# Performance work log

Hardware: AMD Instinct MI355X
Metric: run time of the kernel (lower is better)

The kernel has to match this reference:

```python
import jax, jax.numpy as jnp
import numpy as np

HEADS = 8
DIM_HEAD = 64
MAX_REL = 200  # max_rel_dist


def setup_inputs() -> dict:
    key = jax.random.key(0)
    ks = jax.random.split(key, 5)
    B, N, D = 4, 2048, 512
    x = jax.random.normal(ks[0], (B, N, D), dtype=jnp.float32)
    temporal_mask = jax.random.randint(ks[1], (N, N), 0, 2, dtype=jnp.int32)
    gamma = jnp.ones((D,), jnp.float32)
    beta = jnp.zeros((D,), jnp.float32)
    Wqkv = jax.random.normal(ks[2], (D, 3 * HEADS * DIM_HEAD), dtype=jnp.float32) * 0.02
    Wout = jax.random.normal(ks[3], (HEADS * DIM_HEAD, D), dtype=jnp.float32) * 0.02
    bout = jnp.zeros((D,), jnp.float32)
    rel_table = jax.random.normal(ks[4], (2 * MAX_REL - 1,), dtype=jnp.float32) * 0.02
    return {"x": x, "gamma": gamma, "beta": beta, "Wqkv": Wqkv, "Wout": Wout,
            "bout": bout, "rel_table": rel_table, "temporal_mask": temporal_mask}


def reference(x, gamma, beta, Wqkv, Wout, bout, rel_table, temporal_mask):
    B, N, D = x.shape
    scale = DIM_HEAD ** -0.5
    # LayerNorm
    mu = jnp.mean(x, axis=-1, keepdims=True)
    var = jnp.mean(jnp.square(x - mu), axis=-1, keepdims=True)
    xn = (x - mu) * jax.lax.rsqrt(var + 1e-5) * gamma + beta
    # QKV projection (no bias), split heads: b n (h d) -> b h n d
    qkv = xn @ Wqkv  # [B, N, 3*H*d]
    q, k, v = jnp.split(qkv, 3, axis=-1)
    split = lambda t: t.reshape(B, N, HEADS, DIM_HEAD).transpose(0, 2, 1, 3)
    q, k, v = split(q), split(k), split(v)
    # scores with learned relative-position bias
    dots = jnp.einsum('bhnd,bhmd->bhnm', q, k) * scale  # [B,H,N,N]
    idx = jnp.arange(N)
    rel = jnp.clip(idx[:, None] - idx[None, :], -(MAX_REL - 1), MAX_REL - 1) + MAX_REL - 1
    dots = dots + rel_table[rel][None, None, :, :]
    # temporal mask (0 -> -inf); large negative for grad safety
    dots = jnp.where(temporal_mask[None, None, :, :] == 0, jnp.float32(-1e9), dots)
    attn = jax.nn.softmax(dots, axis=-1)
    out = jnp.einsum('bhnm,bhmd->bhnd', attn, v)
    out = out.transpose(0, 2, 1, 3).reshape(B, N, HEADS * DIM_HEAD)
    return out @ Wout + bout
```

## Files before the change

### kernel.cpp

```cpp
#include <hip/hip_runtime.h>

typedef __attribute__((ext_vector_type(8))) short bf16x8;
typedef __attribute__((ext_vector_type(4))) short bf16x4;
typedef __attribute__((ext_vector_type(4))) float f32x4;
typedef unsigned short ushort_t;

#define B_ 4
#define H_ 8
#define N_ 2048
#define D_ 512
#define MAXREL 199

__device__ __forceinline__ ushort_t f2bf(float f) {
    union { float f; unsigned u; } v; v.f = f;
    unsigned r = v.u + 0x7fffu + ((v.u >> 16) & 1u);
    return (ushort_t)(r >> 16);
}
__device__ __forceinline__ ushort_t f2bf_fast(float f) {
    union { float f; unsigned u; } v; v.f = f;
    return (ushort_t)((v.u + 0x8000u) >> 16);
}
__device__ __forceinline__ float bf2f(ushort_t u) {
    union { unsigned u; float f; } v; v.u = ((unsigned)u) << 16;
    return v.f;
}
__device__ __forceinline__ void gl_lds16(const ushort_t* g, ushort_t* l) {
    __builtin_amdgcn_global_load_lds(
        (const __attribute__((address_space(1))) void*)g,
        (__attribute__((address_space(3))) void*)l,
        16, 0, 0);
}

#define PREP_BIAS  16384
#define PREP_LN    8192
#define PREP_WQ    768
#define PREP_WO    256
__global__ __launch_bounds__(256) void prep_kernel(const float* __restrict__ x,
                                                   const float* __restrict__ gamma,
                                                   const float* __restrict__ beta,
                                                   ushort_t* __restrict__ xn,
                                                   const float* __restrict__ Wqkv,
                                                   ushort_t* __restrict__ WqkvT,
                                                   const float* __restrict__ Wout,
                                                   ushort_t* __restrict__ WoutT,
                                                   const float* __restrict__ rel,
                                                   const int* __restrict__ mask,
                                                   ushort_t* __restrict__ bp) {
    __shared__ float smem[32 * 33];
    const int blk = blockIdx.x;
    const int t = threadIdx.x;

    if (blk < PREP_BIAS) {
        int idx = blk * 256 + t;
        int n = idx >> 11, m = idx & 2047;
        int dl = n - m;
        dl = dl < -MAXREL ? -MAXREL : (dl > MAXREL ? MAXREL : dl);
        float v = (mask[idx] == 0) ? -1e9f : rel[dl + MAXREL];
        int jt = m >> 6, m16 = m & 15, nt = (m >> 4) & 3;
        bp[((size_t)n * 32 + jt) * 64 + m16 * 4 + nt] = f2bf(v);
    } else if (blk < PREP_BIAS + PREP_LN) {
        const int row = blk - PREP_BIAS;
        const float* xr = x + (size_t)row * D_;
        float v0 = xr[t];
        float v1 = xr[t + 256];
        float s = v0 + v1;
        for (int o = 32; o > 0; o >>= 1) s += __shfl_down(s, o);
        if ((t & 63) == 0) smem[t >> 6] = s;
        __syncthreads();
        float mu = (smem[0] + smem[1] + smem[2] + smem[3]) * (1.0f / D_);
        __syncthreads();
        float d0 = v0 - mu, d1 = v1 - mu;
        float s2 = d0 * d0 + d1 * d1;
        for (int o = 32; o > 0; o >>= 1) s2 += __shfl_down(s2, o);
        if ((t & 63) == 0) smem[t >> 6] = s2;
        __syncthreads();
        float var = (smem[0] + smem[1] + smem[2] + smem[3]) * (1.0f / D_);
        float rs = rsqrtf(var + 1e-5f);
        ushort_t* yr = xn + (size_t)row * D_;
        yr[t]       = f2bf(d0 * rs * gamma[t]       + beta[t]);
        yr[t + 256] = f2bf(d1 * rs * gamma[t + 256] + beta[t + 256]);
    } else {
        const float* W; ushort_t* Wt; int Nn, i;
        if (blk < PREP_BIAS + PREP_LN + PREP_WQ) {
            i = blk - (PREP_BIAS + PREP_LN); W = Wqkv; Wt = WqkvT; Nn = 1536;
        } else {
            i = blk - (PREP_BIAS + PREP_LN + PREP_WQ); W = Wout; Wt = WoutT; Nn = 512;
        }
        const int nb = Nn >> 5;
        const int bx = (i % nb) * 32, by = (i / nb) * 32;
        const int tx = t & 31, ty = t >> 5;
        float (*tile)[33] = (float(*)[33])smem;
        #pragma unroll
        for (int k = 0; k < 32; k += 8)
            tile[ty + k][tx] = W[(size_t)(by + ty + k) * Nn + bx + tx];
        __syncthreads();
        #pragma unroll
        for (int k = 0; k < 32; k += 8)
            Wt[(size_t)(bx + ty + k) * 512 + by + tx] = f2bf(tile[tx][ty + k]);
    }
}

__global__ __launch_bounds__(256) void gemm_qkv(const ushort_t* __restrict__ A,
                                                const ushort_t* __restrict__ Bt,
                                                ushort_t* __restrict__ qb,
                                                ushort_t* __restrict__ kb,
                                                ushort_t* __restrict__ vb) {
    __shared__ ushort_t As[128 * 32];
    __shared__ ushort_t Bs[128 * 32];
    const int t = threadIdx.x;
    const int lane = t & 63, w = t >> 6;
    const int m16 = lane & 15, quad = lane >> 4;
    const int wr = w >> 1, wc = w & 1;
    const int r0 = blockIdx.y * 128, c0 = blockIdx.x * 128;

    const ushort_t* Ag = A  + (size_t)(r0 + (t >> 2)) * D_ + (t & 3) * 8;
    const ushort_t* Bg = Bt + (size_t)(c0 + (t >> 2)) * D_ + (t & 3) * 8;
    ushort_t* AsW = As + w * 512;
    ushort_t* BsW = Bs + w * 512;

    f32x4 acc[4][4];
    #pragma unroll
    for (int i = 0; i < 4; i++)
        #pragma unroll
        for (int j = 0; j < 4; j++) acc[i][j] = (f32x4){0.f, 0.f, 0.f, 0.f};

    for (int k0 = 0; k0 < D_; k0 += 32) {
        gl_lds16(Ag + k0, AsW);
        gl_lds16(Ag + k0 + (size_t)64 * D_, AsW + 2048);
        gl_lds16(Bg + k0, BsW);
        gl_lds16(Bg + k0 + (size_t)64 * D_, BsW + 2048);
        __syncthreads();
        bf16x8 af[4], bfr[4];
        #pragma unroll
        for (int rt = 0; rt < 4; rt++)
            af[rt] = *(const bf16x8*)(As + (wr * 64 + rt * 16 + m16) * 32 + quad * 8);
        #pragma unroll
        for (int ct = 0; ct < 4; ct++)
            bfr[ct] = *(const bf16x8*)(Bs + (wc * 64 + ct * 16 + m16) * 32 + quad * 8);
        #pragma unroll
        for (int rt = 0; rt < 4; rt++)
            #pragma unroll
            for (int ct = 0; ct < 4; ct++)
                acc[rt][ct] = __builtin_amdgcn_mfma_f32_16x16x32_bf16(af[rt], bfr[ct], acc[rt][ct], 0, 0, 0);
        __syncthreads();
    }

    #pragma unroll
    for (int ct = 0; ct < 4; ct++) {
        int cc = c0 + wc * 64 + ct * 16;
        int which = cc >> 9;
        int h = (cc >> 6) & 7;
        int d = (cc & 63) + m16;
        #pragma unroll
        for (int rt = 0; rt < 4; rt++) {
            int rowb = r0 + wr * 64 + rt * 16 + quad * 4;
            int b = rowb >> 11, n0 = rowb & 2047;
            if (which == 0) {
                #pragma unroll
                for (int r = 0; r < 4; r++)
                    qb[((size_t)((b * H_ + h) * N_ + n0 + r)) * 64 + d] = f2bf(acc[rt][ct][r] * 0.125f);
            } else if (which == 1) {
                #pragma unroll
                for (int r = 0; r < 4; r++)
                    kb[((size_t)((b * H_ + h) * N_ + n0 + r)) * 64 + d] = f2bf(acc[rt][ct][r]);
            } else {
                union { ushort_t u4[4]; unsigned long long ll; } pk;
                #pragma unroll
                for (int r = 0; r < 4; r++) pk.u4[r] = f2bf(acc[rt][ct][r]);
                *(unsigned long long*)(vb + ((size_t)((b * H_ + h) * 64 + d)) * N_ + n0) = pk.ll;
            }
        }
    }
}

__global__ __launch_bounds__(256) void gemm_out(const ushort_t* __restrict__ A,
                                                const ushort_t* __restrict__ Bt,
                                                const float* __restrict__ bias,
                                                float* __restrict__ C) {
    __shared__ ushort_t As[64 * 32];
    __shared__ ushort_t Bs[128 * 32];
    const int t = threadIdx.x;
    const int lane = t & 63, w = t >> 6;
    const int m16 = lane & 15, quad = lane >> 4;
    const int wr = w >> 1, wc = w & 1;
    const int r0 = blockIdx.y * 64, c0 = blockIdx.x * 128;

    const ushort_t* Ag = A  + (size_t)(r0 + (t >> 2)) * D_ + (t & 3) * 8;
    const ushort_t* Bg = Bt + (size_t)(c0 + (t >> 2)) * D_ + (t & 3) * 8;
    ushort_t* AsW = As + w * 512;
    ushort_t* BsW = Bs + w * 512;

    f32x4 acc[2][4];
    #pragma unroll
    for (int i = 0; i < 2; i++)
        #pragma unroll
        for (int j = 0; j < 4; j++) acc[i][j] = (f32x4){0.f, 0.f, 0.f, 0.f};

    for (int k0 = 0; k0 < D_; k0 += 32) {
        gl_lds16(Ag + k0, AsW);
        gl_lds16(Bg + k0, BsW);
        gl_lds16(Bg + k0 + (size_t)64 * D_, BsW + 2048);
        __syncthreads();
        bf16x8 af[2], bfr[4];
        #pragma unroll
        for (int mf = 0; mf < 2; mf++)
            af[mf] = *(const bf16x8*)(As + (wr * 32 + mf * 16 + m16) * 32 + quad * 8);
        #pragma unroll
        for (int nt = 0; nt < 4; nt++)
            bfr[nt] = *(const bf16x8*)(Bs + (wc * 64 + nt * 16 + m16) * 32 + quad * 8);
        #pragma unroll
        for (int mf = 0; mf < 2; mf++)
            #pragma unroll
            for (int nt = 0; nt < 4; nt++)
                acc[mf][nt] = __builtin_amdgcn_mfma_f32_16x16x32_bf16(af[mf], bfr[nt], acc[mf][nt], 0, 0, 0);
        __syncthreads();
    }

    #pragma unroll
    for (int mf = 0; mf < 2; mf++) {
        #pragma unroll
        for (int nt = 0; nt < 4; nt++) {
            int col = c0 + wc * 64 + nt * 16 + m16;
            int row0 = r0 + wr * 32 + mf * 16 + quad * 4;
            float bv = bias[col];
            #pragma unroll
            for (int r = 0; r < 4; r++)
                C[(size_t)(row0 + r) * 512 + col] = acc[mf][nt][r] + bv;
        }
    }
}

__global__ __launch_bounds__(512, 4) void attn_mfma(const ushort_t* __restrict__ qb,
                                                    const ushort_t* __restrict__ kb,
                                                    const ushort_t* __restrict__ vb,
                                                    const ushort_t* __restrict__ bp,
                                                    ushort_t* __restrict__ attn) {
    __shared__ ushort_t Ks[2][64 * 64];
    __shared__ ushort_t Vs[2][64 * 64];
    __shared__ ushort_t p_s[8][16 * 64];

    const int t = threadIdx.x;
    const int w = t >> 6, lane = t & 63;
    const int m16 = lane & 15, quad = lane >> 4;
    const int id = blockIdx.x;
    const int bh = id & 31;
    const int qt = id >> 5;
    const int b = bh >> 3, h = bh & 7;
    const int n0w = qt * 128 + w * 16;

    const int srow = t >> 3, scb = t & 7;
    const int soff = srow * 64 + (scb ^ (srow & 7)) * 8;
    const ushort_t* kgbase = kb + ((size_t)bh * N_) * 64;
    const ushort_t* vgbase = vb + ((size_t)bh * 64) * N_;

    const ushort_t* qpb = qb + ((size_t)(bh * N_ + n0w + m16)) * 64 + quad * 8;
    bf16x8 qa0 = *(const bf16x8*)(qpb);
    bf16x8 qa1 = *(const bf16x8*)(qpb + 32);

    *(bf16x8*)(&Ks[0][soff]) = *(const bf16x8*)(kgbase + (size_t)srow * 64 + scb * 8);
    *(bf16x8*)(&Vs[0][soff]) = *(const bf16x8*)(vgbase + (size_t)srow * N_ + scb * 8);
    __syncthreads();

    f32x4 o[4];
    #pragma unroll
    for (int nt = 0; nt < 4; nt++) o[nt] = (f32x4){0.f, 0.f, 0.f, 0.f};
    float rsum[4] = {};

    for (int jt = 0; jt < 32; jt++) {
        const int buf = jt & 1;
        const int j0 = jt * 64;
        const bool more = (jt < 31);

        bf16x8 kst, vst;
        if (more) {
            kst = *(const bf16x8*)(kgbase + (size_t)(j0 + 64 + srow) * 64 + scb * 8);
            vst = *(const bf16x8*)(vgbase + (size_t)srow * N_ + j0 + 64 + scb * 8);
        }

        bf16x4 bcur[4];
        #pragma unroll
        for (int r = 0; r < 4; r++) {
            int n = n0w + quad * 4 + r;
            bcur[r] = *(const bf16x4*)(bp + ((size_t)n * 32 + jt) * 64 + m16 * 4);
        }

        f32x4 s[4];
        #pragma unroll
        for (int nt = 0; nt < 4; nt++) {
            int kr = nt * 16 + m16;
            bf16x8 kf0 = *(const bf16x8*)(&Ks[buf][kr * 64 + ((quad) ^ (kr & 7)) * 8]);
            bf16x8 kf1 = *(const bf16x8*)(&Ks[buf][kr * 64 + ((quad + 4) ^ (kr & 7)) * 8]);
            f32x4 a2 = (f32x4){0.f, 0.f, 0.f, 0.f};
            a2 = __builtin_amdgcn_mfma_f32_16x16x32_bf16(qa0, kf0, a2, 0, 0, 0);
            a2 = __builtin_amdgcn_mfma_f32_16x16x32_bf16(qa1, kf1, a2, 0, 0, 0);
            s[nt] = a2;
        }

        ushort_t* pw = p_s[w];
        #pragma unroll
        for (int nt = 0; nt < 4; nt++) {
            int chunk = nt * 2 + (m16 >> 3), pos = m16 & 7;
            #pragma unroll
            for (int r = 0; r < 4; r++) {
                float p = __expf(s[nt][r] + bf2f((ushort_t)bcur[r][nt]));
                rsum[r] += p;
                int row = quad * 4 + r;
                pw[row * 64 + ((chunk ^ (row & 7)) << 3) + pos] = f2bf_fast(p);
            }
        }

        bf16x8 pa0 = *(const bf16x8*)(pw + m16 * 64 + ((quad ^ (m16 & 7)) << 3));
        bf16x8 pa1 = *(const bf16x8*)(pw + m16 * 64 + (((quad + 4) ^ (m16 & 7)) << 3));

        #pragma unroll
        for (int nt = 0; nt < 4; nt++) {
            int d = nt * 16 + m16;
            bf16x8 vf0 = *(const bf16x8*)(&Vs[buf][d * 64 + ((quad) ^ (d & 7)) * 8]);
            bf16x8 vf1 = *(const bf16x8*)(&Vs[buf][d * 64 + ((quad + 4) ^ (d & 7)) * 8]);
            o[nt] = __builtin_amdgcn_mfma_f32_16x16x32_bf16(pa0, vf0, o[nt], 0, 0, 0);
            o[nt] = __builtin_amdgcn_mfma_f32_16x16x32_bf16(pa1, vf1, o[nt], 0, 0, 0);
        }

        if (more) {
            *(bf16x8*)(&Ks[buf ^ 1][soff]) = kst;
            *(bf16x8*)(&Vs[buf ^ 1][soff]) = vst;
        }
        __syncthreads();
    }

    #pragma unroll
    for (int r = 0; r < 4; r++) {
        float t2 = rsum[r];
        t2 += __shfl_xor(t2, 1);
        t2 += __shfl_xor(t2, 2);
        t2 += __shfl_xor(t2, 4);
        t2 += __shfl_xor(t2, 8);
        float inv = 1.0f / t2;
        int n = n0w + quad * 4 + r;
        ushort_t* orow = attn + ((size_t)(b * N_ + n)) * 512 + h * 64 + m16;
        #pragma unroll
        for (int nt = 0; nt < 4; nt++) orow[nt * 16] = f2bf(o[nt][r] * inv);
    }
}

extern "C" void kernel_launch(void* const* d_in, const int* in_sizes, int n_in,
                              void* d_out, int out_size, void* d_ws, size_t ws_size,
                              hipStream_t stream) {
    const float* x     = (const float*)d_in[0];
    const float* gamma = (const float*)d_in[1];
    const float* beta  = (const float*)d_in[2];
    const float* Wqkv  = (const float*)d_in[3];
    const float* Wout  = (const float*)d_in[4];
    const float* bout  = (const float*)d_in[5];
    const float* rel   = (const float*)d_in[6];
    const int*   mask  = (const int*)d_in[7];
    float* out = (float*)d_out;

    char* wsb = (char*)d_ws;
    ushort_t* xn    = (ushort_t*)(wsb);
    ushort_t* attnb = (ushort_t*)(wsb + ( 8u << 20));
    ushort_t* qb    = (ushort_t*)(wsb + (16u << 20));
    ushort_t* kb    = (ushort_t*)(wsb + (24u << 20));
    ushort_t* vb    = (ushort_t*)(wsb + (32u << 20));
    ushort_t* WqkvT = (ushort_t*)(wsb + (40u << 20));
    ushort_t* WoutT = (ushort_t*)(wsb + (42u << 20));
    ushort_t* bp    = (ushort_t*)(wsb + (44u << 20));

    prep_kernel<<<PREP_BIAS + PREP_LN + PREP_WQ + PREP_WO, 256, 0, stream>>>(
        x, gamma, beta, xn, Wqkv, WqkvT, Wout, WoutT, rel, mask, bp);

    gemm_qkv<<<dim3(1536 / 128, 8192 / 128), 256, 0, stream>>>(xn, WqkvT, qb, kb, vb);

    attn_mfma<<<512, 512, 0, stream>>>(qb, kb, vb, bp, attnb);

    gemm_out<<<dim3(512 / 128, 8192 / 64), 256, 0, stream>>>(attnb, WoutT, bout, out);
}
```

Measured before the change: 198.6 us.

## Compute transposed scores, pass probabilities via shuffles instead of LDS, use exp2

After: 210.6 us. 6.1% more time.

```diff
diff --git a/kernel.cpp b/kernel.cpp
--- a/kernel.cpp
+++ b/kernel.cpp
@@ -10,19 +10,28 @@
 #define N_ 2048
 #define D_ 512
 #define MAXREL 199
+#define LOG2E 1.4426950408889634f
 
 __device__ __forceinline__ ushort_t f2bf(float f) {
     union { float f; unsigned u; } v; v.f = f;
     unsigned r = v.u + 0x7fffu + ((v.u >> 16) & 1u);
     return (ushort_t)(r >> 16);
 }
-__device__ __forceinline__ ushort_t f2bf_fast(float f) {
-    union { float f; unsigned u; } v; v.f = f;
-    return (ushort_t)((v.u + 0x8000u) >> 16);
-}
 __device__ __forceinline__ float bf2f(ushort_t u) {
     union { unsigned u; float f; } v; v.u = ((unsigned)u) << 16;
     return v.f;
+}
+__device__ __forceinline__ float fexp2(float x) {
+#if __has_builtin(__builtin_amdgcn_exp2f)
+    return __builtin_amdgcn_exp2f(x);
+#else
+    return __expf(x * 0.6931471805599453f);
+#endif
+}
+__device__ __forceinline__ unsigned cvt_pk_bf16(float lo, float hi) {
+    unsigned r;
+    asm("v_cvt_pk_bf16_f32 %0, %1, %2" : "=v"(r) : "v"(lo), "v"(hi));
+    return r;
 }
 __device__ __forceinline__ void gl_lds16(const ushort_t* g, ushort_t* l) {
     __builtin_amdgcn_global_load_lds(
@@ -55,9 +64,8 @@
         int n = idx >> 11, m = idx & 2047;
         int dl = n - m;
         dl = dl < -MAXREL ? -MAXREL : (dl > MAXREL ? MAXREL : dl);
-        float v = (mask[idx] == 0) ? -1e9f : rel[dl + MAXREL];
-        int jt = m >> 6, m16 = m & 15, nt = (m >> 4) & 3;
-        bp[((size_t)n * 32 + jt) * 64 + m16 * 4 + nt] = f2bf(v);
+        float v = (mask[idx] == 0) ? -1e9f : rel[dl + MAXREL] * LOG2E;
+        bp[idx] = f2bf(v);
     } else if (blk < PREP_BIAS + PREP_LN) {
         const int row = blk - PREP_BIAS;
         const float* xr = x + (size_t)row * D_;
@@ -158,7 +166,7 @@
             if (which == 0) {
                 #pragma unroll
                 for (int r = 0; r < 4; r++)
-                    qb[((size_t)((b * H_ + h) * N_ + n0 + r)) * 64 + d] = f2bf(acc[rt][ct][r] * 0.125f);
+                    qb[((size_t)((b * H_ + h) * N_ + n0 + r)) * 64 + d] = f2bf(acc[rt][ct][r] * (0.125f * LOG2E));
             } else if (which == 1) {
                 #pragma unroll
                 for (int r = 0; r < 4; r++)
@@ -237,7 +245,6 @@
                                                     ushort_t* __restrict__ attn) {
     __shared__ ushort_t Ks[2][64 * 64];
     __shared__ ushort_t Vs[2][64 * 64];
-    __shared__ ushort_t p_s[8][16 * 64];
 
     const int t = threadIdx.x;
     const int w = t >> 6, lane = t & 63;
@@ -257,6 +264,12 @@
     bf16x8 qa0 = *(const bf16x8*)(qpb);
     bf16x8 qa1 = *(const bf16x8*)(qpb + 32);
 
+    const ushort_t* bprow = bp + (size_t)(n0w + m16) * 2048 + quad * 4;
+
+    const int srcA = m16 + 32 * (quad & 1);
+    const int srcB = srcA + 16;
+    const bool lowhalf = (quad < 2);
+
     *(bf16x8*)(&Ks[0][soff]) = *(const bf16x8*)(kgbase + (size_t)srow * 64 + scb * 8);
     *(bf16x8*)(&Vs[0][soff]) = *(const bf16x8*)(vgbase + (size_t)srow * N_ + scb * 8);
     __syncthreads();
@@ -264,7 +277,7 @@
     f32x4 o[4];
     #pragma unroll
     for (int nt = 0; nt < 4; nt++) o[nt] = (f32x4){0.f, 0.f, 0.f, 0.f};
-    float rsum[4] = {};
+    float rsum = 0.f;
 
     for (int jt = 0; jt < 32; jt++) {
         const int buf = jt & 1;
@@ -277,48 +290,57 @@
             vst = *(const bf16x8*)(vgbase + (size_t)srow * N_ + j0 + 64 + scb * 8);
         }
 
-        bf16x4 bcur[4];
-        #pragma unroll
-        for (int r = 0; r < 4; r++) {
-            int n = n0w + quad * 4 + r;
-            bcur[r] = *(const bf16x4*)(bp + ((size_t)n * 32 + jt) * 64 + m16 * 4);
-        }
-
-        f32x4 s[4];
+        bf16x4 bc[4];
+        #pragma unroll
+        for (int nt = 0; nt < 4; nt++) bc[nt] = *(const bf16x4*)(bprow + jt * 64 + nt * 16);
+
+        unsigned pk[8];
         #pragma unroll
         for (int nt = 0; nt < 4; nt++) {
+            f32x4 a2;
+            #pragma unroll
+            for (int r = 0; r < 4; r++) a2[r] = bf2f((ushort_t)bc[nt][r]);
             int kr = nt * 16 + m16;
             bf16x8 kf0 = *(const bf16x8*)(&Ks[buf][kr * 64 + ((quad) ^ (kr & 7)) * 8]);
             bf16x8 kf1 = *(const bf16x8*)(&Ks[buf][kr * 64 + ((quad + 4) ^ (kr & 7)) * 8]);
-            f32x4 a2 = (f32x4){0.f, 0.f, 0.f, 0.f};
-            a2 = __builtin_amdgcn_mfma_f32_16x16x32_bf16(qa0, kf0, a2, 0, 0, 0);
-            a2 = __builtin_amdgcn_mfma_f32_16x16x32_bf16(qa1, kf1, a2, 0, 0, 0);
-            s[nt] = a2;
-        }
-
-        ushort_t* pw = p_s[w];
-        #pragma unroll
-        for (int nt = 0; nt < 4; nt++) {
-            int chunk = nt * 2 + (m16 >> 3), pos = m16 & 7;
-            #pragma unroll
-            for (int r = 0; r < 4; r++) {
-                float p = __expf(s[nt][r] + bf2f((ushort_t)bcur[r][nt]));
-                rsum[r] += p;
-                int row = quad * 4 + r;
-                pw[row * 64 + ((chunk ^ (row & 7)) << 3) + pos] = f2bf_fast(p);
-            }
-        }
-
-        bf16x8 pa0 = *(const bf16x8*)(pw + m16 * 64 + ((quad ^ (m16 & 7)) << 3));
-        bf16x8 pa1 = *(const bf16x8*)(pw + m16 * 64 + (((quad + 4) ^ (m16 & 7)) << 3));
+            a2 = __builtin_amdgcn_mfma_f32_16x16x32_bf16(kf0, qa0, a2, 0, 0, 0);
+            a2 = __builtin_amdgcn_mfma_f32_16x16x32_bf16(kf1, qa1, a2, 0, 0, 0);
+            float p0 = fexp2(a2[0]);
+            float p1 = fexp2(a2[1]);
+            float p2 = fexp2(a2[2]);
+            float p3 = fexp2(a2[3]);
+            rsum += (p0 + p1) + (p2 + p3);
+            pk[nt * 2]     = cvt_pk_bf16(p0, p1);
+            pk[nt * 2 + 1] = cvt_pk_bf16(p2, p3);
+        }
+
+        union { unsigned u[4]; bf16x8 v; } pa0u, pa1u;
+        {
+            unsigned e0 = __shfl(pk[0], srcA), o0 = __shfl(pk[2], srcA);
+            unsigned e1 = __shfl(pk[1], srcA), o1 = __shfl(pk[3], srcA);
+            unsigned e2 = __shfl(pk[0], srcB), o2 = __shfl(pk[2], srcB);
+            unsigned e3 = __shfl(pk[1], srcB), o3 = __shfl(pk[3], srcB);
+            pa0u.u[0] = lowhalf ? e0 : o0;
+            pa0u.u[1] = lowhalf ? e1 : o1;
+            pa0u.u[2] = lowhalf ? e2 : o2;
+            pa0u.u[3] = lowhalf ? e3 : o3;
+            unsigned f0 = __shfl(pk[4], srcA), g0 = __shfl(pk[6], srcA);
+            unsigned f1 = __shfl(pk[5], srcA), g1 = __shfl(pk[7], srcA);
+            unsigned f2 = __shfl(pk[4], srcB), g2 = __shfl(pk[6], srcB);
+            unsigned f3 = __shfl(pk[5], srcB), g3 = __shfl(pk[7], srcB);
+            pa1u.u[0] = lowhalf ? f0 : g0;
+            pa1u.u[1] = lowhalf ? f1 : g1;
+            pa1u.u[2] = lowhalf ? f2 : g2;
+            pa1u.u[3] = lowhalf ? f3 : g3;
+        }
 
         #pragma unroll
         for (int nt = 0; nt < 4; nt++) {
             int d = nt * 16 + m16;
             bf16x8 vf0 = *(const bf16x8*)(&Vs[buf][d * 64 + ((quad) ^ (d & 7)) * 8]);
             bf16x8 vf1 = *(const bf16x8*)(&Vs[buf][d * 64 + ((quad + 4) ^ (d & 7)) * 8]);
-            o[nt] = __builtin_amdgcn_mfma_f32_16x16x32_bf16(pa0, vf0, o[nt], 0, 0, 0);
-            o[nt] = __builtin_amdgcn_mfma_f32_16x16x32_bf16(pa1, vf1, o[nt], 0, 0, 0);
+            o[nt] = __builtin_amdgcn_mfma_f32_16x16x32_bf16(pa0u.v, vf0, o[nt], 0, 0, 0);
+            o[nt] = __builtin_amdgcn_mfma_f32_16x16x32_bf16(pa1u.v, vf1, o[nt], 0, 0, 0);
         }
 
         if (more) {
@@ -328,14 +350,12 @@
         __syncthreads();
     }
 
+    rsum += __shfl_xor(rsum, 16);
+    rsum += __shfl_xor(rsum, 32);
+
     #pragma unroll
     for (int r = 0; r < 4; r++) {
-        float t2 = rsum[r];
-        t2 += __shfl_xor(t2, 1);
-        t2 += __shfl_xor(t2, 2);
-        t2 += __shfl_xor(t2, 4);
-        t2 += __shfl_xor(t2, 8);
-        float inv = 1.0f / t2;
+        float inv = 1.0f / __shfl(rsum, quad * 4 + r);
         int n = n0w + quad * 4 + r;
         ushort_t* orow = attn + ((size_t)(b * N_ + n)) * 512 + h * 64 + m16;
         #pragma unroll
```
